# Kernel tuning notes

Measured on AMD Instinct MI355X. Metric: run time of the kernel, lower is better.

Reference implementation:

```python
import jax, jax.numpy as jnp
import numpy as np

N_NODES = 50000
N_EDGES = 800000
D_IN = 64
D_HID = 64
N_GRAPHS = 64


def setup_inputs() -> dict:
    key = jax.random.key(0)
    ks = jax.random.split(key, 10)
    x = jax.random.normal(ks[0], (N_NODES, D_IN), dtype=jnp.float32)
    edge_index = jax.random.randint(ks[1], (2, N_EDGES), 0, N_NODES, dtype=jnp.int64)
    batch = jnp.sort(jax.random.randint(ks[2], (N_NODES,), 0, N_GRAPHS, dtype=jnp.int64))
    s1 = 1.0 / np.sqrt(D_IN)
    s2 = 1.0 / np.sqrt(D_HID)
    W1 = jax.random.uniform(ks[3], (D_IN, D_HID), jnp.float32, -s1, s1)
    b1 = jnp.zeros((D_HID,), jnp.float32)
    W2 = jax.random.uniform(ks[4], (D_HID, D_HID), jnp.float32, -s2, s2)
    b2 = jnp.zeros((D_HID,), jnp.float32)
    W3 = jax.random.uniform(ks[5], (D_HID, D_HID), jnp.float32, -s2, s2)
    b3 = jnpp = jnp.zeros((D_HID,), jnp.float32)
    return {"x": x, "edge_index": edge_index, "batch": batch,
            "W1": W1, "b1": b1, "W2": W2, "b2": b2, "W3": W3, "b3": b3}


def _gcn_norm(edge_index, num_nodes):
    # add self-loops, then symmetric normalization deg^-1/2 A_hat deg^-1/2
    loop = jnp.arange(num_nodes, dtype=edge_index.dtype)
    row = jnp.concatenate([edge_index[0], loop])  # source
    col = jnp.concatenate([edge_index[1], loop])  # target (aggregation index)
    deg = jax.ops.segment_sum(jnp.ones_like(col, dtype=jnp.float32), col,
                              num_segments=num_nodes)
    dinv = jnp.where(deg > 0, jax.lax.rsqrt(deg), 0.0)
    norm = dinv[row] * dinv[col]  # [E+N]
    return row, col, norm


def _gcn_conv(x, row, col, norm, W, b, num_nodes):
    h = x @ W                                   # [N, D] small GEMM
    msg = h[row] * norm[:, None]                # edge-wise gather + scale
    out = jax.ops.segment_sum(msg, col, num_segments=num_nodes)  # scatter-add
    return out + b


def reference(x, edge_index, batch, W1, b1, W2, b2, W3, b3):
    n = x.shape[0]
    row, col, norm = _gcn_norm(edge_index, n)
    h = jax.nn.relu(_gcn_conv(x, row, col, norm, W1, b1, n))
    h = jax.nn.relu(_gcn_conv(h, row, col, norm, W2, b2, n))
    h = jax.nn.relu(_gcn_conv(h, row, col, norm, W3, b3, n))
    # global_mean_pool over graphs
    sums = jax.ops.segment_sum(h, batch, num_segments=N_GRAPHS)
    cnt = jax.ops.segment_sum(jnp.ones((n,), jnp.float32), batch,
                              num_segments=N_GRAPHS)
    return sums / jnp.maximum(cnt, 1.0)[:, None]
```

## Files before the change

### kernel.cpp

```cpp
#include <hip/hip_runtime.h>

#define N_NODES   50000
#define N_EDGES   800000
#define DF        64
#define N_GRAPHS  64
#define NPAD      50176

#define ABLK 200
#define AEDG (N_EDGES/ABLK)
#define RSH  9
#define NREG 98
#define RPAD 128
#define CAP  12288

__global__ __launch_bounds__(256)
void k_hist(const int* __restrict__ col, int* __restrict__ H,
            float* __restrict__ pool) {
    __shared__ int h[RPAD];
    const int t = threadIdx.x, b = blockIdx.x;
    if (b == 0)
        for (int i = t; i < N_GRAPHS * DF; i += 256) pool[i] = 0.f;
    if (t < RPAD) h[t] = 0;
    __syncthreads();
    const int e0 = b * AEDG;
    for (int i = t; i < AEDG; i += 256)
        atomicAdd(&h[col[e0 + i] >> RSH], 1);
    __syncthreads();
    if (t < RPAD) H[t * ABLK + b] = h[t];
}

__global__ __launch_bounds__(256)
void k_scanH(const int* __restrict__ H, int* __restrict__ O,
             int* __restrict__ T) {
    __shared__ int s[256];
    const int t = threadIdx.x, r = blockIdx.x;
    int v = (t < ABLK) ? H[r * ABLK + t] : 0;
    s[t] = v; __syncthreads();
    #pragma unroll
    for (int off = 1; off < 256; off <<= 1) {
        int x = (t >= off) ? s[t - off] : 0;
        __syncthreads();
        s[t] += x;
        __syncthreads();
    }
    if (t < ABLK) O[r * ABLK + t] = s[t] - v;
    if (t == 255) T[r] = s[255];
}

__global__ __launch_bounds__(256)
void k_bin(const int* __restrict__ row, const int* __restrict__ col,
           const int* __restrict__ O, const int* __restrict__ T,
           unsigned* __restrict__ staging) {
    __shared__ int cur[RPAD];
    __shared__ int rs[RPAD];
    const int t = threadIdx.x, b = blockIdx.x;
    int v = 0;
    if (t < RPAD) { v = T[t]; rs[t] = v; }
    __syncthreads();
    #pragma unroll
    for (int off = 1; off < RPAD; off <<= 1) {
        int x = 0;
        if (t < RPAD && t >= off) x = rs[t - off];
        __syncthreads();
        if (t < RPAD) rs[t] += x;
        __syncthreads();
    }
    if (t < RPAD) cur[t] = O[t * ABLK + b] + (rs[t] - v);
    __syncthreads();
    const int e0 = b * AEDG;
    for (int i = t; i < AEDG; i += 256) {
        int c = col[e0 + i];
        int rr = row[e0 + i];
        int slot = atomicAdd(&cur[c >> RSH], 1);
        staging[slot] = ((unsigned)c << 16) | (unsigned)rr;
    }
}

__global__ __launch_bounds__(512)
void k_csr(const unsigned* __restrict__ staging, const int* __restrict__ T,
           int* __restrict__ offs, float* __restrict__ dinv,
           unsigned* __restrict__ epack) {
    __shared__ int hist[512];
    __shared__ int cur[512];
    __shared__ unsigned img[CAP];
    __shared__ int rs[RPAD];
    __shared__ int sh_s0, sh_s1;
    const int t = threadIdx.x, r = blockIdx.x;
    int v = 0;
    if (t < RPAD) { v = T[t]; rs[t] = v; }
    __syncthreads();
    #pragma unroll
    for (int off = 1; off < RPAD; off <<= 1) {
        int x = 0;
        if (t < RPAD && t >= off) x = rs[t - off];
        __syncthreads();
        if (t < RPAD) rs[t] += x;
        __syncthreads();
    }
    if (t == r) { sh_s0 = rs[t] - v; sh_s1 = rs[t]; }
    hist[t] = 0;
    __syncthreads();
    const int s0 = sh_s0, s1 = sh_s1;
    for (int i = s0 + t; i < s1; i += 512) {
        int ln = (int)(staging[i] >> 16) - (r << RSH);
        atomicAdd(&hist[ln], 1);
    }
    __syncthreads();
    int myc = hist[t];
    #pragma unroll
    for (int off = 1; off < 512; off <<= 1) {
        int x = (t >= off) ? hist[t - off] : 0;
        __syncthreads();
        hist[t] += x;
        __syncthreads();
    }
    int excl = hist[t] - myc;
    int n = (r << RSH) + t;
    offs[n] = s0 + excl;
    if (n < N_NODES) dinv[n] = rsqrtf((float)(myc + 1));
    cur[t] = excl;
    __syncthreads();
    for (int i = s0 + t; i < s1; i += 512) {
        unsigned p = staging[i];
        int ln = (int)(p >> 16) - (r << RSH);
        unsigned rr = p & 0xFFFFu;
        unsigned pk = rr | ((unsigned)ln << 16);
        int slot = atomicAdd(&cur[ln], 1);
        if (slot < CAP) img[slot] = pk;
        else           epack[s0 + slot] = pk;
    }
    __syncthreads();
    int cnt = s1 - s0; if (cnt > CAP) cnt = CAP;
    for (int j = t; j < cnt; j += 512) epack[s0 + j] = img[j];
}

__global__ __launch_bounds__(256)
void k_scale(const float* __restrict__ x, const float* __restrict__ dinv,
             float* __restrict__ hs) {
    int i = blockIdx.x * blockDim.x + threadIdx.x;
    if (i < N_NODES * DF / 4) {
        int n = (i * 4) >> 6;
        float s = dinv[n];
        float4 v = ((const float4*)x)[i];
        v.x *= s; v.y *= s; v.z *= s; v.w *= s;
        ((float4*)hs)[i] = v;
    }
}

#define FB_ROWS 64
#define LDX 68
#define ECAP 2048

__global__ __launch_bounds__(512, 8)
void k_fused(const int* __restrict__ offs, const unsigned* __restrict__ epack,
             const float* __restrict__ dinv, const float* __restrict__ hs,
             const float* __restrict__ W, const float* __restrict__ bias,
             float* __restrict__ out, const int* __restrict__ batch,
             float* __restrict__ pool) {
    __shared__ float  XsT[DF][LDX];
    __shared__ float  Ws[DF][DF];
    __shared__ unsigned short es_l[ECAP];
    __shared__ int    s_offs[FB_ROWS + 1];
    __shared__ float  plocal[4 * DF];
    __shared__ int    sh_batch[FB_ROWS];

    const int t = threadIdx.x;
    const int row0 = blockIdx.x * FB_ROWS;

    for (int idx = t * 4; idx < DF * DF; idx += 512 * 4) {
        float4 w = *(const float4*)&W[idx];
        Ws[idx >> 6][(idx & 63) + 0] = w.x;
        Ws[idx >> 6][(idx & 63) + 1] = w.y;
        Ws[idx >> 6][(idx & 63) + 2] = w.z;
        Ws[idx >> 6][(idx & 63) + 3] = w.w;
    }
    if (t <= FB_ROWS) s_offs[t] = offs[row0 + t];
    if (pool) {
        if (t < 4 * DF) plocal[t] = 0.f;
        if (t < FB_ROWS) {
            int n = row0 + t;
            sh_batch[t] = batch[n < N_NODES ? n : N_NODES - 1];
        }
    }
    __syncthreads();

    const int eb  = s_offs[0];
    const int cnt = s_offs[FB_ROWS] - eb;
    const int lim = cnt < ECAP ? cnt : ECAP;
    for (int i = t; i < lim; i += 512)
        es_l[i] = (unsigned short)(epack[eb + i] & 0xFFFFu);
    __syncthreads();

    const int wv = t >> 6;
    const int l  = t & 63;
    const int ng = l >> 4;
    const int q4 = (l & 15) << 2;

    for (int set = 0; set < 2; ++set) {
        const int r = (wv << 3) + (set << 2) + ng;
        const int n = row0 + r;
        const float dc = (n < N_NODES) ? dinv[n] : 0.f;
        const unsigned hn = (n < N_NODES) ? (unsigned)n : 0u;

        float4 acc = *(const float4*)&hs[(hn << 6) + q4];

        int s        = s_offs[r]     - eb;
        const int s1 = s_offs[r + 1] - eb;
        while (s < s1) {
            unsigned srcs[8];
            #pragma unroll
            for (int k = 0; k < 8; ++k) {
                const int li = s + k;
                unsigned sr = hn;
                if (li < s1)
                    sr = (li < ECAP) ? (unsigned)es_l[li]
                                     : (epack[eb + li] & 0xFFFFu);
                srcs[k] = (li < s1) ? sr : hn;
            }
            float4 v[8];
            #pragma unroll
            for (int k = 0; k < 8; ++k)
                v[k] = *(const float4*)&hs[(srcs[k] << 6) + q4];
            #pragma unroll
            for (int k = 0; k < 8; ++k) {
                const int li = s + k;
                const float m = (li < s1) ? 1.f : 0.f;
                acc.x += m * v[k].x; acc.y += m * v[k].y;
                acc.z += m * v[k].z; acc.w += m * v[k].w;
            }
            s += 8;
        }

        XsT[q4 + 0][r] = acc.x * dc;
        XsT[q4 + 1][r] = acc.y * dc;
        XsT[q4 + 2][r] = acc.z * dc;
        XsT[q4 + 3][r] = acc.w * dc;
    }
    __syncthreads();

    const int i = (t & 15) * 4;
    const int j = (t >> 4) * 2;
    float acc[4][2] = {};
    #pragma unroll 8
    for (int k = 0; k < DF; ++k) {
        float4 xv = *(const float4*)&XsT[k][i];
        float2 wvv = *(const float2*)&Ws[k][j];
        acc[0][0] += xv.x * wvv.x; acc[0][1] += xv.x * wvv.y;
        acc[1][0] += xv.y * wvv.x; acc[1][1] += xv.y * wvv.y;
        acc[2][0] += xv.z * wvv.x; acc[2][1] += xv.z * wvv.y;
        acc[3][0] += xv.w * wvv.x; acc[3][1] += xv.w * wvv.y;
    }
    const float bx = bias[j], by = bias[j + 1];

    if (!pool) {
        #pragma unroll
        for (int u = 0; u < 4; ++u) {
            int gr = row0 + i + u;
            if (gr < N_NODES) {
                float sc = dinv[gr];
                float ox = acc[u][0] + bx;
                float oy = acc[u][1] + by;
                ox = ox > 0.f ? ox : 0.f;
                oy = oy > 0.f ? oy : 0.f;
                *(float2*)&out[gr * DF + j] = make_float2(ox * sc, oy * sc);
            }
        }
    } else {
        const int g0 = sh_batch[0];
        const int span = sh_batch[FB_ROWS - 1] - g0 + 1;
        if (span <= 4) {
            #pragma unroll
            for (int u = 0; u < 4; ++u) {
                int gr = row0 + i + u;
                if (gr < N_NODES) {
                    float ox = acc[u][0] + bx;
                    float oy = acc[u][1] + by;
                    ox = ox > 0.f ? ox : 0.f;
                    oy = oy > 0.f ? oy : 0.f;
                    int gl = sh_batch[i + u] - g0;
                    atomicAdd(&plocal[gl * DF + j],     ox);
                    atomicAdd(&plocal[gl * DF + j + 1], oy);
                }
            }
            __syncthreads();
            for (int idx = t; idx < span * DF; idx += 512)
                atomicAdd(&pool[g0 * DF + idx], plocal[idx]);
        } else {
            #pragma unroll
            for (int u = 0; u < 4; ++u) {
                int gr = row0 + i + u;
                if (gr < N_NODES) {
                    float ox = acc[u][0] + bx;
                    float oy = acc[u][1] + by;
                    ox = ox > 0.f ? ox : 0.f;
                    oy = oy > 0.f ? oy : 0.f;
                    int gg = sh_batch[i + u];
                    atomicAdd(&pool[gg * DF + j],     ox);
                    atomicAdd(&pool[gg * DF + j + 1], oy);
                }
            }
        }
    }
}

__device__ __forceinline__ int lb(const int* a, int n, int key) {
    int lo = 0, hi = n;
    while (lo < hi) { int m = (lo + hi) >> 1; if (a[m] < key) lo = m + 1; else hi = m; }
    return lo;
}

__global__ void k_div(const float* __restrict__ pool, const int* __restrict__ batch,
                      float* __restrict__ out) {
    int idx = blockIdx.x * blockDim.x + threadIdx.x;
    if (idx < N_GRAPHS * DF) {
        int g = idx >> 6;
        int c = lb(batch, N_NODES, g + 1) - lb(batch, N_NODES, g);
        out[idx] = pool[idx] / fmaxf((float)c, 1.0f);
    }
}


extern "C" void kernel_launch(void* const* d_in, const int* in_sizes, int n_in,
                              void* d_out, int out_size, void* d_ws, size_t ws_size,
                              hipStream_t stream) {
    const float* x     = (const float*)d_in[0];
    const int*   ei    = (const int*)d_in[1];
    const int*   batch = (const int*)d_in[2];
    const float* W1    = (const float*)d_in[3];
    const float* b1    = (const float*)d_in[4];
    const float* W2    = (const float*)d_in[5];
    const float* b2    = (const float*)d_in[6];
    const float* W3    = (const float*)d_in[7];
    const float* b3    = (const float*)d_in[8];
    float* out = (float*)d_out;

    const int* row = ei;
    const int* col = ei + N_EDGES;

    char* wsb = (char*)d_ws;
    float*    pool    = (float*)wsb;
    int*      H       = (int*)(pool + N_GRAPHS * DF);
    int*      O       = H + RPAD * ABLK;
    int*      T       = O + RPAD * ABLK;
    int*      offs    = T + RPAD;
    unsigned* epack   = (unsigned*)(offs + NPAD);
    unsigned* staging = epack + N_EDGES;
    float*    dinv    = (float*)(staging + N_EDGES);
    float*    bufA    = dinv + NPAD;
    float*    bufB    = bufA + N_NODES * DF;

    const int nblk_F = (N_NODES + FB_ROWS - 1) / FB_ROWS;
    const int nblk_S = (N_NODES * DF / 4 + 255) / 256;

    k_hist<<<ABLK, 256, 0, stream>>>(col, H, pool);
    k_scanH<<<RPAD, 256, 0, stream>>>(H, O, T);
    k_bin<<<ABLK, 256, 0, stream>>>(row, col, O, T, staging);
    k_csr<<<NREG, 512, 0, stream>>>(staging, T, offs, dinv, epack);

    k_scale<<<nblk_S, 256, 0, stream>>>(x, dinv, bufB);

    k_fused<<<nblk_F, 512, 0, stream>>>(offs, epack, dinv, bufB, W1, b1, bufA,
                                        nullptr, nullptr);
    k_fused<<<nblk_F, 512, 0, stream>>>(offs, epack, dinv, bufA, W2, b2, bufB,
                                        nullptr, nullptr);
    k_fused<<<nblk_F, 512, 0, stream>>>(offs, epack, dinv, bufB, W3, b3, nullptr,
                                        batch, pool);

    k_div<<<(N_GRAPHS * DF + 255) / 256, 256, 0, stream>>>(pool, batch, out);
}
```

Measured before the change: 245.1 us.

## Double fused GCN block threads and halve per-thread feature width

Raises the fused aggregation+GEMM kernel from 512 to 1024 threads per block. Each lane now gathers a float2 slice instead of a float4, so 32 lanes cover a node row. Each thread computes one output column for 4 rows in the GEMM. The edge gather is also split into a shared-memory path and a global-memory fallback, chosen per block by whether the edge count fits ECAP, which removes a per-edge branch. The aim is more parallelism and memory-level parallelism for the random row gathers, at the cost of narrower loads, more index work per byte and possibly lower occupancy with 1024-thread blocks.

```diff
diff --git a/kernel.cpp b/kernel.cpp
--- a/kernel.cpp
+++ b/kernel.cpp
@@ -151,7 +151,7 @@
 #define LDX 68
 #define ECAP 2048
 
-__global__ __launch_bounds__(512, 8)
+__global__ __launch_bounds__(1024, 8)
 void k_fused(const int* __restrict__ offs, const unsigned* __restrict__ epack,
              const float* __restrict__ dinv, const float* __restrict__ hs,
              const float* __restrict__ W, const float* __restrict__ bias,
@@ -167,12 +167,15 @@
     const int t = threadIdx.x;
     const int row0 = blockIdx.x * FB_ROWS;
 
-    for (int idx = t * 4; idx < DF * DF; idx += 512 * 4) {
-        float4 w = *(const float4*)&W[idx];
-        Ws[idx >> 6][(idx & 63) + 0] = w.x;
-        Ws[idx >> 6][(idx & 63) + 1] = w.y;
-        Ws[idx >> 6][(idx & 63) + 2] = w.z;
-        Ws[idx >> 6][(idx & 63) + 3] = w.w;
+    {
+        int idx = t * 4;
+        if (idx < DF * DF) {
+            float4 w = *(const float4*)&W[idx];
+            Ws[idx >> 6][(idx & 63) + 0] = w.x;
+            Ws[idx >> 6][(idx & 63) + 1] = w.y;
+            Ws[idx >> 6][(idx & 63) + 2] = w.z;
+            Ws[idx >> 6][(idx & 63) + 3] = w.w;
+        }
     }
     if (t <= FB_ROWS) s_offs[t] = offs[row0 + t];
     if (pool) {
@@ -186,84 +189,91 @@
 
     const int eb  = s_offs[0];
     const int cnt = s_offs[FB_ROWS] - eb;
-    const int lim = cnt < ECAP ? cnt : ECAP;
-    for (int i = t; i < lim; i += 512)
-        es_l[i] = (unsigned short)(epack[eb + i] & 0xFFFFu);
+    if (cnt <= ECAP)
+        for (int i = t; i < cnt; i += 1024)
+            es_l[i] = (unsigned short)(epack[eb + i] & 0xFFFFu);
     __syncthreads();
 
     const int wv = t >> 6;
     const int l  = t & 63;
-    const int ng = l >> 4;
-    const int q4 = (l & 15) << 2;
+    const int ng = l >> 5;
+    const int q2 = (l & 31) << 1;
 
     for (int set = 0; set < 2; ++set) {
-        const int r = (wv << 3) + (set << 2) + ng;
+        const int r = (wv << 2) + (set << 1) + ng;
         const int n = row0 + r;
         const float dc = (n < N_NODES) ? dinv[n] : 0.f;
         const unsigned hn = (n < N_NODES) ? (unsigned)n : 0u;
 
-        float4 acc = *(const float4*)&hs[(hn << 6) + q4];
+        float2 acc = *(const float2*)&hs[(hn << 6) + q2];
 
         int s        = s_offs[r]     - eb;
         const int s1 = s_offs[r + 1] - eb;
-        while (s < s1) {
-            unsigned srcs[8];
-            #pragma unroll
-            for (int k = 0; k < 8; ++k) {
-                const int li = s + k;
-                unsigned sr = hn;
-                if (li < s1)
-                    sr = (li < ECAP) ? (unsigned)es_l[li]
-                                     : (epack[eb + li] & 0xFFFFu);
-                srcs[k] = (li < s1) ? sr : hn;
+        if (cnt <= ECAP) {
+            while (s < s1) {
+                unsigned srcs[8];
+                #pragma unroll
+                for (int k = 0; k < 8; ++k) {
+                    const int li = s + k;
+                    srcs[k] = (li < s1) ? (unsigned)es_l[li] : hn;
+                }
+                float2 v[8];
+                #pragma unroll
+                for (int k = 0; k < 8; ++k)
+                    v[k] = *(const float2*)&hs[(srcs[k] << 6) + q2];
+                #pragma unroll
+                for (int k = 0; k < 8; ++k) {
+                    const float m = (s + k < s1) ? 1.f : 0.f;
+                    acc.x += m * v[k].x; acc.y += m * v[k].y;
+                }
+                s += 8;
             }
-            float4 v[8];
-            #pragma unroll
-            for (int k = 0; k < 8; ++k)
-                v[k] = *(const float4*)&hs[(srcs[k] << 6) + q4];
-            #pragma unroll
-            for (int k = 0; k < 8; ++k) {
-                const int li = s + k;
-                const float m = (li < s1) ? 1.f : 0.f;
-                acc.x += m * v[k].x; acc.y += m * v[k].y;
-                acc.z += m * v[k].z; acc.w += m * v[k].w;
+        } else {
+            while (s < s1) {
+                unsigned srcs[8];
+                #pragma unroll
+                for (int k = 0; k < 8; ++k) {
+                    const int li = s + k;
+                    srcs[k] = (li < s1) ? (epack[eb + li] & 0xFFFFu) : hn;
+                }
+                float2 v[8];
+                #pragma unroll
+                for (int k = 0; k < 8; ++k)
+                    v[k] = *(const float2*)&hs[(srcs[k] << 6) + q2];
+                #pragma unroll
+                for (int k = 0; k < 8; ++k) {
+                    const float m = (s + k < s1) ? 1.f : 0.f;
+                    acc.x += m * v[k].x; acc.y += m * v[k].y;
+                }
+                s += 8;
             }
-            s += 8;
-        }
-
-        XsT[q4 + 0][r] = acc.x * dc;
-        XsT[q4 + 1][r] = acc.y * dc;
-        XsT[q4 + 2][r] = acc.z * dc;
-        XsT[q4 + 3][r] = acc.w * dc;
+        }
+
+        XsT[q2 + 0][r] = acc.x * dc;
+        XsT[q2 + 1][r] = acc.y * dc;
     }
     __syncthreads();
 
     const int i = (t & 15) * 4;
-    const int j = (t >> 4) * 2;
-    float acc[4][2] = {};
+    const int j = (t >> 4) & 63;
+    float a0 = 0.f, a1 = 0.f, a2 = 0.f, a3 = 0.f;
     #pragma unroll 8
     for (int k = 0; k < DF; ++k) {
         float4 xv = *(const float4*)&XsT[k][i];
-        float2 wvv = *(const float2*)&Ws[k][j];
-        acc[0][0] += xv.x * wvv.x; acc[0][1] += xv.x * wvv.y;
-        acc[1][0] += xv.y * wvv.x; acc[1][1] += xv.y * wvv.y;
-        acc[2][0] += xv.z * wvv.x; acc[2][1] += xv.z * wvv.y;
-        acc[3][0] += xv.w * wvv.x; acc[3][1] += xv.w * wvv.y;
-    }
-    const float bx = bias[j], by = bias[j + 1];
+        float w = Ws[k][j];
+        a0 += xv.x * w; a1 += xv.y * w; a2 += xv.z * w; a3 += xv.w * w;
+    }
+    const float bb = bias[j];
+    float o[4] = { a0 + bb, a1 + bb, a2 + bb, a3 + bb };
+    #pragma unroll
+    for (int u = 0; u < 4; ++u) o[u] = o[u] > 0.f ? o[u] : 0.f;
 
     if (!pool) {
         #pragma unroll
         for (int u = 0; u < 4; ++u) {
             int gr = row0 + i + u;
-            if (gr < N_NODES) {
-                float sc = dinv[gr];
-                float ox = acc[u][0] + bx;
-                float oy = acc[u][1] + by;
-                ox = ox > 0.f ? ox : 0.f;
-                oy = oy > 0.f ? oy : 0.f;
-                *(float2*)&out[gr * DF + j] = make_float2(ox * sc, oy * sc);
-            }
+            if (gr < N_NODES)
+                out[gr * DF + j] = o[u] * dinv[gr];
         }
     } else {
         const int g0 = sh_batch[0];
@@ -273,30 +283,20 @@
             for (int u = 0; u < 4; ++u) {
                 int gr = row0 + i + u;
                 if (gr < N_NODES) {
-                    float ox = acc[u][0] + bx;
-                    float oy = acc[u][1] + by;
-                    ox = ox > 0.f ? ox : 0.f;
-                    oy = oy > 0.f ? oy : 0.f;
                     int gl = sh_batch[i + u] - g0;
-                    atomicAdd(&plocal[gl * DF + j],     ox);
-                    atomicAdd(&plocal[gl * DF + j + 1], oy);
+                    atomicAdd(&plocal[gl * DF + j], o[u]);
                 }
             }
             __syncthreads();
-            for (int idx = t; idx < span * DF; idx += 512)
+            for (int idx = t; idx < span * DF; idx += 1024)
                 atomicAdd(&pool[g0 * DF + idx], plocal[idx]);
         } else {
             #pragma unroll
             for (int u = 0; u < 4; ++u) {
                 int gr = row0 + i + u;
                 if (gr < N_NODES) {
-                    float ox = acc[u][0] + bx;
-                    float oy = acc[u][1] + by;
-                    ox = ox > 0.f ? ox : 0.f;
-                    oy = oy > 0.f ? oy : 0.f;
                     int gg = sh_batch[i + u];
-                    atomicAdd(&pool[gg * DF + j],     ox);
-                    atomicAdd(&pool[gg * DF + j + 1], oy);
+                    atomicAdd(&pool[gg * DF + j], o[u]);
                 }
             }
         }
@@ -359,12 +359,12 @@
 
     k_scale<<<nblk_S, 256, 0, stream>>>(x, dinv, bufB);
 
-    k_fused<<<nblk_F, 512, 0, stream>>>(offs, epack, dinv, bufB, W1, b1, bufA,
-                                        nullptr, nullptr);
-    k_fused<<<nblk_F, 512, 0, stream>>>(offs, epack, dinv, bufA, W2, b2, bufB,
-                                        nullptr, nullptr);
-    k_fused<<<nblk_F, 512, 0, stream>>>(offs, epack, dinv, bufB, W3, b3, nullptr,
-                                        batch, pool);
+    k_fused<<<nblk_F, 1024, 0, stream>>>(offs, epack, dinv, bufB, W1, b1, bufA,
+                                         nullptr, nullptr);
+    k_fused<<<nblk_F, 1024, 0, stream>>>(offs, epack, dinv, bufA, W2, b2, bufB,
+                                         nullptr, nullptr);
+    k_fused<<<nblk_F, 1024, 0, stream>>>(offs, epack, dinv, bufB, W3, b3, nullptr,
+                                         batch, pool);
 
     k_div<<<(N_GRAPHS * DF + 255) / 256, 256, 0, stream>>>(pool, batch, out);
 }
```

Measured after the change: 275.6 us. +12.4%, slower.
